# Kernel optimization log

Measured on AMD Instinct MI355X. Metric: run time of the kernel, lower is better.

The kernel has to match this reference:

```python
import jax, jax.numpy as jnp
import numpy as np

NEG = -100000000.0  # NOT_POSSIBLE_TRANSITION
B, T, F, NT = 64, 512, 1024, 50
H = NT + 2  # +2 for start/stop tags
START, STOP = H - 2, H - 1


def setup_inputs() -> dict:
    key = jax.random.key(0)
    k0, k1, k2, k3 = jax.random.split(key, 4)
    features = jax.random.normal(k0, (B, T, F), jnp.float32)
    tags = jax.random.randint(k1, (B, T), 0, NT)
    masks = jnp.ones((B, T), jnp.float32)
    W = jax.random.normal(k2, (H, F), jnp.float32) * 0.02  # nn.Linear weight
    b = jnp.zeros((H,), jnp.float32)                        # nn.Linear bias
    transition = jax.random.normal(k3, (H, H), jnp.float32)
    transition = transition.at[START, :].set(NEG).at[:, STOP].set(NEG)
    return dict(features=features, W=W, b=b, transition=transition,
                masks=masks, tags=tags)


def _forward_algorithm(emit, masks, transition):
    # emit: [B,T,H], masks: [B,T]
    b_, _, h = emit.shape
    init = jnp.full((b_, h), NEG, emit.dtype).at[:, START].set(0.0)

    def step(scores, xs):
        emit_t, mask_t = xs  # [B,H], [B]
        # score_t[b, i] = logsumexp_j(scores[b,j] + transition[i,j] + emit_t[b,i])
        s = scores[:, None, :] + transition[None, :, :] + emit_t[:, :, None]
        s = jax.nn.logsumexp(s, axis=-1)
        m = mask_t[:, None]
        scores = s * m + scores * (1.0 - m)
        return scores, None

    scores, _ = jax.lax.scan(step, init, (emit.transpose(1, 0, 2), masks.T))
    return jax.nn.logsumexp(scores + transition[STOP], axis=-1)  # [B]


def _gold_score(emit, tags, masks, transition):
    b_ = emit.shape[0]
    emit_sc = jnp.take_along_axis(emit, tags[:, :, None], axis=2)[:, :, 0]  # [B,T]
    start = jnp.full((b_, 1), START, tags.dtype)
    tags_ext = jnp.concatenate([start, tags], axis=1)  # [B,T+1]
    trans_sc = transition[tags_ext[:, 1:], tags_ext[:, :-1]]  # [B,T]
    last_pos = masks.sum(axis=1).astype(jnp.int32)  # index into tags_ext
    last_tag = jnp.take_along_axis(tags_ext, last_pos[:, None], axis=1)[:, 0]
    last_score = transition[STOP, last_tag]
    return ((trans_sc + emit_sc) * masks).sum(axis=1) + last_score  # [B]


def reference(features, W, b, transition, masks, tags):
    emit = features @ W.T + b  # [B,T,H]
    fwd = _forward_algorithm(emit, masks, transition)
    gold = _gold_score(emit, tags, masks, transition)
    return (fwd - gold).mean()  # CRF NLL loss (scalar)


if __name__ == "__main__":
    print(reference(**setup_inputs()))
```

## Files before the change

kernel.cpp:

```cpp
#include <hip/hip_runtime.h>
#include <hip/hip_bf16.h>
#include <math.h>


#define NEGV   (-100000000.0f)
#define BB     64
#define TT     512
#define FF     1024
#define HH     52
#define HP     64
#define S_START 50
#define S_STOP  51
#define NCH    32
#define CLEN   (TT / NCH)

typedef __bf16 bf16x8 __attribute__((ext_vector_type(8)));
typedef __bf16 bf16x4 __attribute__((ext_vector_type(4)));
typedef float  f32x4  __attribute__((ext_vector_type(4)));

#define WS_CHUNK  0u
#define WS_WBF    33554432u
#define WS_EXPT   33685504u
#define WS_GOLD   33693696u
#define WS_CEXP   33693952u

__global__ __launch_bounds__(256) void k_prep(const float* __restrict__ W,
                                              const float* __restrict__ trans,
                                              __bf16* __restrict__ wbf,
                                              __bf16* __restrict__ expT,
                                              float* __restrict__ gold) {
  int n = blockIdx.x;
  if (n == 0) {
    if (threadIdx.x < BB) gold[threadIdx.x] = 0.0f;
    for (int idx = threadIdx.x; idx < 4096; idx += 256) {
      int m = idx >> 6, k = idx & 63;
      float tv = (k >= HH) ? NEGV : ((m >= HH) ? 0.0f : trans[m * HH + k]);
      expT[idx] = (__bf16)__expf(tv);
    }
  }
  for (int k = threadIdx.x; k < FF; k += 256) {
    float v = (n < HH) ? W[n * FF + k] : 0.0f;
    wbf[n * FF + k] = (__bf16)v;
  }
}

__global__ __launch_bounds__(256, 2) void k_scan(const float* __restrict__ feat,
                                                 const __bf16* __restrict__ wbf,
                                                 const __bf16* __restrict__ expT,
                                                 const float* __restrict__ bias,
                                                 const float* __restrict__ trans,
                                                 const float* __restrict__ masks,
                                                 const int* __restrict__ tags,
                                                 __bf16* __restrict__ chunks,
                                                 float* __restrict__ cexp,
                                                 float* __restrict__ gold) {
  const int tid = threadIdx.x;
  const int wv = tid >> 6;
  const int l  = tid & 63;
  const int lm = l & 15;
  const int q  = l >> 4;
  const int chunk = blockIdx.x * 4 + wv;
  const int b = chunk >> 5, c = chunk & 31;

  __shared__ __align__(16) __bf16 PTall[4][64 * 72];
  __shared__ __align__(16) __bf16 Eall[4][CLEN * 64];
  __bf16* pt = PTall[wv];
  __bf16* el = Eall[wv];

  const float* fbase = feat + ((size_t)(b * TT + c * CLEN)) * FF;
  const float* arow  = fbase + (size_t)lm * FF + q * 8;

  f32x4 apre[4][2];
#pragma unroll
  for (int s = 0; s < 4; ++s)
#pragma unroll
    for (int h = 0; h < 2; ++h)
      apre[s][h] = *(const f32x4*)(arow + s * 32 + h * 4);

  bf16x8 bcur[4];
#pragma unroll
  for (int nt = 0; nt < 4; ++nt)
    bcur[nt] = *(const bf16x8*)(wbf + (size_t)(nt * 16 + lm) * FF + q * 8);

  f32x4 acc[4] = {};

#pragma unroll
  for (int kt = 0; kt < 32; ++kt) {
    const int st = kt & 3;
    bf16x8 af;
#pragma unroll
    for (int j = 0; j < 4; ++j) {
      af[j]     = (__bf16)apre[st][0][j];
      af[4 + j] = (__bf16)apre[st][1][j];
    }
    if (kt + 4 < 32) {
#pragma unroll
      for (int h = 0; h < 2; ++h)
        apre[st][h] = *(const f32x4*)(arow + (kt + 4) * 32 + h * 4);
    }
    bf16x8 bnx[4];
    if (kt + 1 < 32) {
#pragma unroll
      for (int nt = 0; nt < 4; ++nt)
        bnx[nt] = *(const bf16x8*)(wbf + (size_t)(nt * 16 + lm) * FF + (kt + 1) * 32 + q * 8);
    }
#pragma unroll
    for (int nt = 0; nt < 4; ++nt)
      acc[nt] = __builtin_amdgcn_mfma_f32_16x16x32_bf16(af, bcur[nt], acc[nt], 0, 0, 0);
    if (kt + 1 < 32) {
#pragma unroll
      for (int nt = 0; nt < 4; ++nt) bcur[nt] = bnx[nt];
    }
  }

#pragma unroll
  for (int nt = 0; nt < 4; ++nt) {
    int n = nt * 16 + lm;
    float bn = (n < HH) ? bias[n] : 0.0f;
#pragma unroll
    for (int rr = 0; rr < 4; ++rr)
      el[(q * 4 + rr) * 64 + n] = (__bf16)(acc[nt][rr] + bn);
  }

  float mreg = (l < CLEN) ? masks[b * TT + c * CLEN + l] : 1.0f;
  int cur = (l < CLEN) ? tags[b * TT + c * CLEN + l] : 0;
  int prev = __shfl_up(cur, 1);
  if (l == 0) prev = (c == 0) ? S_START : tags[b * TT + c * CLEN - 1];
  float gp = 0.0f;
  if (l < CLEN) {
    float e  = (float)el[l * 64 + cur];
    float tr = trans[cur * HH + prev];
    gp = (e + tr) * mreg;
  }
#pragma unroll
  for (int d = 1; d < 64; d <<= 1) gp += __shfl_xor(gp, d);
  if (l == 0) atomicAdd(&gold[b], gp);

  bf16x8 afrag[4][2];
#pragma unroll
  for (int mt = 0; mt < 4; ++mt)
#pragma unroll
    for (int kk = 0; kk < 2; ++kk)
      afrag[mt][kk] = *(const bf16x8*)&expT[(mt * 16 + lm) * 64 + kk * 32 + q * 8];

  for (int idx = l; idx < 4096; idx += 64) {
    int n = idx >> 6, mm = idx & 63;
    pt[n * 72 + mm] = (__bf16)((n == mm) ? 1.0f : 0.0f);
  }

  int eacc = 0, rpend = 0;
  const float LOG2E = 1.4426950408889634f;

  for (int t = 0; t < CLEN; ++t) {
    float mcur = __shfl(mreg, t);
    if (mcur != 0.0f) {
      float sh = (float)(7 + rpend);
      eacc += 7 + rpend;
      rpend = 0;
      float s[4][4];
#pragma unroll
      for (int mt = 0; mt < 4; ++mt) {
        bf16x4 em4 = *(const bf16x4*)&el[t * 64 + mt * 16 + q * 4];
#pragma unroll
        for (int rr = 0; rr < 4; ++rr)
          s[mt][rr] = __builtin_amdgcn_exp2f(fmaf((float)em4[rr], LOG2E, -sh));
      }

      bf16x8 bfr[2][4];
#pragma unroll
      for (int kk = 0; kk < 2; ++kk)
#pragma unroll
        for (int nt = 0; nt < 4; ++nt)
          bfr[kk][nt] = *(const bf16x8*)&pt[(nt * 16 + lm) * 72 + kk * 32 + q * 8];

      const bool trk = ((t & 7) == 7) && (t != CLEN - 1);
      float lmax = 0.0f;
      f32x4 zero = {};
#pragma unroll
      for (int mt = 0; mt < 4; ++mt) {
#pragma unroll
        for (int nt = 0; nt < 4; ++nt) {
          f32x4 a = __builtin_amdgcn_mfma_f32_16x16x32_bf16(afrag[mt][0], bfr[0][nt], zero, 0, 0, 0);
          a = __builtin_amdgcn_mfma_f32_16x16x32_bf16(afrag[mt][1], bfr[1][nt], a, 0, 0, 0);
          bf16x4 w4;
#pragma unroll
          for (int rr = 0; rr < 4; ++rr) {
            float v = a[rr] * s[mt][rr];
            if (trk) lmax = fmaxf(lmax, v);
            w4[rr] = (__bf16)v;
          }
          *(bf16x4*)&pt[(nt * 16 + lm) * 72 + mt * 16 + q * 4] = w4;
        }
      }
      if (trk) {
#pragma unroll
        for (int d = 1; d < 64; d <<= 1) lmax = fmaxf(lmax, __shfl_xor(lmax, d));
        rpend = ilogbf(lmax);
      }
    }
  }

  __bf16* cb = chunks + (size_t)chunk * 4096;
#pragma unroll
  for (int it = 0; it < 8; ++it) {
    bf16x8 v;
#pragma unroll
    for (int e = 0; e < 8; ++e) v[e] = pt[(it * 8 + e) * 72 + l];
    *(bf16x8*)&cb[it * 512 + l * 8] = v;
  }
  if (l == 0) cexp[chunk] = (float)eacc;
}

__global__ __launch_bounds__(64) void k_combine(const __bf16* __restrict__ chunks,
                                                const float* __restrict__ cexp,
                                                const float* __restrict__ trans,
                                                const float* __restrict__ masks,
                                                const int* __restrict__ tags,
                                                const float* __restrict__ gold,
                                                float* __restrict__ out) {
  const int b = blockIdx.x;
  const int l = threadIdx.x;
  __shared__ __align__(16) float vsh[64];
  float v = (l == S_START) ? 1.0f : 0.0f;
  float esum = 0.0f;
  const float LN2 = 0.6931471805599453f;

  float msum = 0.0f;
  for (int t = l; t < TT; t += 64) msum += masks[b * TT + t];

  const __bf16* base = chunks + ((size_t)(b * NCH)) * 4096;

  bf16x8 pf[4][8];
#pragma unroll
  for (int p = 0; p < 4; ++p)
#pragma unroll
    for (int it = 0; it < 8; ++it)
      pf[p][it] = *(const bf16x8*)&base[(size_t)p * 4096 + it * 512 + l * 8];

#pragma unroll
  for (int cc = 0; cc < NCH; ++cc) {
    vsh[l] = v;
    __syncthreads();
    float u = 0.0f;
#pragma unroll
    for (int it = 0; it < 8; ++it) {
      bf16x8 m8 = pf[cc & 3][it];
      f32x4 va = *(const f32x4*)&vsh[it * 8];
      f32x4 vb = *(const f32x4*)&vsh[it * 8 + 4];
      u += (float)m8[0] * va[0] + (float)m8[1] * va[1]
         + (float)m8[2] * va[2] + (float)m8[3] * va[3]
         + (float)m8[4] * vb[0] + (float)m8[5] * vb[1]
         + (float)m8[6] * vb[2] + (float)m8[7] * vb[3];
    }
    if (cc + 4 < NCH) {
#pragma unroll
      for (int it = 0; it < 8; ++it)
        pf[cc & 3][it] = *(const bf16x8*)&base[(size_t)(cc + 4) * 4096 + it * 512 + l * 8];
    }
    esum += cexp[b * NCH + cc] * LN2;
    float mxx = u;
#pragma unroll
    for (int d = 1; d < 64; d <<= 1) mxx = fmaxf(mxx, __shfl_xor(mxx, d));
    if (mxx > 0.0f) {
      int ee = ilogbf(mxx);
      u = ldexpf(u, -ee);
      esum += (float)ee * LN2;
    }
    v = u;
    __syncthreads();
  }

  float ts = (l < HH) ? trans[S_STOP * HH + l] : NEGV;
  float contrib = v * __expf(ts);
#pragma unroll
  for (int d = 1; d < 64; d <<= 1) {
    contrib += __shfl_xor(contrib, d);
    msum += __shfl_xor(msum, d);
  }
  if (l == 0) {
    int lp = (int)(msum + 0.5f);
    int lt = (lp == 0) ? S_START : tags[b * TT + lp - 1];
    float goldb = gold[b] + trans[S_STOP * HH + lt];
    float fwd = __logf(contrib) + esum;
    atomicAdd(out, (fwd - goldb) * (1.0f / 64.0f));
  }
}

extern "C" void kernel_launch(void* const* d_in, const int* in_sizes, int n_in,
                              void* d_out, int out_size, void* d_ws, size_t ws_size,
                              hipStream_t stream) {
  (void)in_sizes; (void)n_in; (void)out_size; (void)ws_size;
  const float* feat  = (const float*)d_in[0];
  const float* W     = (const float*)d_in[1];
  const float* bias  = (const float*)d_in[2];
  const float* trans = (const float*)d_in[3];
  const float* masks = (const float*)d_in[4];
  const int*   tags  = (const int*)d_in[5];

  char* ws = (char*)d_ws;
  __bf16* chunks = (__bf16*)(ws + WS_CHUNK);
  __bf16* wbf    = (__bf16*)(ws + WS_WBF);
  __bf16* expT   = (__bf16*)(ws + WS_EXPT);
  float*  gold   = (float*)(ws + WS_GOLD);
  float*  cexp   = (float*)(ws + WS_CEXP);

  hipMemsetAsync(d_out, 0, sizeof(float), stream);
  k_prep<<<HP, 256, 0, stream>>>(W, trans, wbf, expT, gold);
  k_scan<<<(BB * NCH) / 4, 256, 0, stream>>>(feat, wbf, expT, bias, trans, masks,
                                             tags, chunks, cexp, gold);
  k_combine<<<BB, 64, 0, stream>>>(chunks, cexp, trans, masks, tags, gold, (float*)d_out);
}
```

Before: 269.2 us.

## Split each scan chunk across two waves in K and in transfer-matrix columns

Each chunk is now processed by two wavefronts instead of one. They split the feature GEMM along K and reduce the partial sums through shared memory. In the chunk scan each wave owns half of the columns of the transfer-matrix product. Each half keeps its own exponent accumulator, and the combine kernel reconciles the two exponents per chunk by rescaling the vector. This doubles the parallelism and halves the serial per-wave work for the latency-bound scan, at the cost of extra barriers, a renormalisation only at t==7, and possibly more range risk in the bf16 products.

```diff
diff --git a/kernel.cpp b/kernel.cpp
--- a/kernel.cpp
+++ b/kernel.cpp
@@ -19,10 +19,10 @@
 typedef float  f32x4  __attribute__((ext_vector_type(4)));
 
 #define WS_CHUNK  0u
-#define WS_WBF    33554432u
-#define WS_EXPT   33685504u
-#define WS_GOLD   33693696u
-#define WS_CEXP   33693952u
+#define WS_CEXP2  16777216u
+#define WS_WBF    16793600u
+#define WS_EXPT   16924672u
+#define WS_GOLD   16932864u
 
 __global__ __launch_bounds__(256) void k_prep(const float* __restrict__ W,
                                               const float* __restrict__ trans,
@@ -44,7 +44,7 @@
   }
 }
 
-__global__ __launch_bounds__(256, 2) void k_scan(const float* __restrict__ feat,
+__global__ __launch_bounds__(256, 4) void k_scan(const float* __restrict__ feat,
                                                  const __bf16* __restrict__ wbf,
                                                  const __bf16* __restrict__ expT,
                                                  const float* __restrict__ bias,
@@ -52,40 +52,43 @@
                                                  const float* __restrict__ masks,
                                                  const int* __restrict__ tags,
                                                  __bf16* __restrict__ chunks,
-                                                 float* __restrict__ cexp,
+                                                 float* __restrict__ cexp2,
                                                  float* __restrict__ gold) {
   const int tid = threadIdx.x;
   const int wv = tid >> 6;
   const int l  = tid & 63;
   const int lm = l & 15;
   const int q  = l >> 4;
-  const int chunk = blockIdx.x * 4 + wv;
+  const int ck = wv >> 1;
+  const int h  = wv & 1;
+  const int chunk = blockIdx.x * 2 + ck;
   const int b = chunk >> 5, c = chunk & 31;
 
-  __shared__ __align__(16) __bf16 PTall[4][64 * 72];
-  __shared__ __align__(16) __bf16 Eall[4][CLEN * 64];
-  __bf16* pt = PTall[wv];
-  __bf16* el = Eall[wv];
+  __shared__ __align__(16) __bf16 PTall[2][64 * 72];
+  __shared__ __align__(16) __bf16 Eall[2][CLEN * 64];
+  __bf16* pt = PTall[ck];
+  __bf16* el = Eall[ck];
+  float*  pstage = (float*)pt;
 
   const float* fbase = feat + ((size_t)(b * TT + c * CLEN)) * FF;
-  const float* arow  = fbase + (size_t)lm * FF + q * 8;
+  const float* arow  = fbase + (size_t)lm * FF + h * 512 + q * 8;
 
   f32x4 apre[4][2];
 #pragma unroll
   for (int s = 0; s < 4; ++s)
 #pragma unroll
-    for (int h = 0; h < 2; ++h)
-      apre[s][h] = *(const f32x4*)(arow + s * 32 + h * 4);
+    for (int hh = 0; hh < 2; ++hh)
+      apre[s][hh] = *(const f32x4*)(arow + s * 32 + hh * 4);
 
   bf16x8 bcur[4];
 #pragma unroll
   for (int nt = 0; nt < 4; ++nt)
-    bcur[nt] = *(const bf16x8*)(wbf + (size_t)(nt * 16 + lm) * FF + q * 8);
+    bcur[nt] = *(const bf16x8*)(wbf + (size_t)(nt * 16 + lm) * FF + h * 512 + q * 8);
 
   f32x4 acc[4] = {};
 
 #pragma unroll
-  for (int kt = 0; kt < 32; ++kt) {
+  for (int kt = 0; kt < 16; ++kt) {
     const int st = kt & 3;
     bf16x8 af;
 #pragma unroll
@@ -93,48 +96,58 @@
       af[j]     = (__bf16)apre[st][0][j];
       af[4 + j] = (__bf16)apre[st][1][j];
     }
-    if (kt + 4 < 32) {
-#pragma unroll
-      for (int h = 0; h < 2; ++h)
-        apre[st][h] = *(const f32x4*)(arow + (kt + 4) * 32 + h * 4);
+    if (kt + 4 < 16) {
+#pragma unroll
+      for (int hh = 0; hh < 2; ++hh)
+        apre[st][hh] = *(const f32x4*)(arow + (kt + 4) * 32 + hh * 4);
     }
     bf16x8 bnx[4];
-    if (kt + 1 < 32) {
+    if (kt + 1 < 16) {
 #pragma unroll
       for (int nt = 0; nt < 4; ++nt)
-        bnx[nt] = *(const bf16x8*)(wbf + (size_t)(nt * 16 + lm) * FF + (kt + 1) * 32 + q * 8);
+        bnx[nt] = *(const bf16x8*)(wbf + (size_t)(nt * 16 + lm) * FF + h * 512 + (kt + 1) * 32 + q * 8);
     }
 #pragma unroll
     for (int nt = 0; nt < 4; ++nt)
       acc[nt] = __builtin_amdgcn_mfma_f32_16x16x32_bf16(af, bcur[nt], acc[nt], 0, 0, 0);
-    if (kt + 1 < 32) {
+    if (kt + 1 < 16) {
 #pragma unroll
       for (int nt = 0; nt < 4; ++nt) bcur[nt] = bnx[nt];
     }
   }
 
 #pragma unroll
-  for (int nt = 0; nt < 4; ++nt) {
-    int n = nt * 16 + lm;
-    float bn = (n < HH) ? bias[n] : 0.0f;
+  for (int nt = 0; nt < 4; ++nt)
 #pragma unroll
     for (int rr = 0; rr < 4; ++rr)
-      el[(q * 4 + rr) * 64 + n] = (__bf16)(acc[nt][rr] + bn);
-  }
+      pstage[h * 1024 + (q * 4 + rr) * 64 + nt * 16 + lm] = acc[nt][rr];
+  __syncthreads();
+
+  {
+    float bl = (l < HH) ? bias[l] : 0.0f;
+#pragma unroll
+    for (int i2 = 0; i2 < 8; ++i2) {
+      int t = i2 * 2 + h;
+      el[t * 64 + l] = (__bf16)(pstage[t * 64 + l] + pstage[1024 + t * 64 + l] + bl);
+    }
+  }
+  __syncthreads();
 
   float mreg = (l < CLEN) ? masks[b * TT + c * CLEN + l] : 1.0f;
-  int cur = (l < CLEN) ? tags[b * TT + c * CLEN + l] : 0;
-  int prev = __shfl_up(cur, 1);
-  if (l == 0) prev = (c == 0) ? S_START : tags[b * TT + c * CLEN - 1];
-  float gp = 0.0f;
-  if (l < CLEN) {
-    float e  = (float)el[l * 64 + cur];
-    float tr = trans[cur * HH + prev];
-    gp = (e + tr) * mreg;
-  }
-#pragma unroll
-  for (int d = 1; d < 64; d <<= 1) gp += __shfl_xor(gp, d);
-  if (l == 0) atomicAdd(&gold[b], gp);
+  if (h == 0) {
+    int cur = (l < CLEN) ? tags[b * TT + c * CLEN + l] : 0;
+    int prev = __shfl_up(cur, 1);
+    if (l == 0) prev = (c == 0) ? S_START : tags[b * TT + c * CLEN - 1];
+    float gp = 0.0f;
+    if (l < CLEN) {
+      float e  = (float)el[l * 64 + cur];
+      float tr = trans[cur * HH + prev];
+      gp = (e + tr) * mreg;
+    }
+#pragma unroll
+    for (int d = 1; d < 64; d <<= 1) gp += __shfl_xor(gp, d);
+    if (l == 0) atomicAdd(&gold[b], gp);
+  }
 
   bf16x8 afrag[4][2];
 #pragma unroll
@@ -143,9 +156,10 @@
     for (int kk = 0; kk < 2; ++kk)
       afrag[mt][kk] = *(const bf16x8*)&expT[(mt * 16 + lm) * 64 + kk * 32 + q * 8];
 
-  for (int idx = l; idx < 4096; idx += 64) {
-    int n = idx >> 6, mm = idx & 63;
-    pt[n * 72 + mm] = (__bf16)((n == mm) ? 1.0f : 0.0f);
+#pragma unroll
+  for (int r = 0; r < 32; ++r) {
+    int j = h * 32 + r;
+    pt[j * 72 + l] = (__bf16)((j == l) ? 1.0f : 0.0f);
   }
 
   int eacc = 0, rpend = 0;
@@ -166,20 +180,20 @@
           s[mt][rr] = __builtin_amdgcn_exp2f(fmaf((float)em4[rr], LOG2E, -sh));
       }
 
-      bf16x8 bfr[2][4];
+      bf16x8 bfr[2][2];
 #pragma unroll
       for (int kk = 0; kk < 2; ++kk)
 #pragma unroll
-        for (int nt = 0; nt < 4; ++nt)
-          bfr[kk][nt] = *(const bf16x8*)&pt[(nt * 16 + lm) * 72 + kk * 32 + q * 8];
-
-      const bool trk = ((t & 7) == 7) && (t != CLEN - 1);
+        for (int nt = 0; nt < 2; ++nt)
+          bfr[kk][nt] = *(const bf16x8*)&pt[((h * 2 + nt) * 16 + lm) * 72 + kk * 32 + q * 8];
+
+      const bool trk = (t == 7);
       float lmax = 0.0f;
       f32x4 zero = {};
 #pragma unroll
       for (int mt = 0; mt < 4; ++mt) {
 #pragma unroll
-        for (int nt = 0; nt < 4; ++nt) {
+        for (int nt = 0; nt < 2; ++nt) {
           f32x4 a = __builtin_amdgcn_mfma_f32_16x16x32_bf16(afrag[mt][0], bfr[0][nt], zero, 0, 0, 0);
           a = __builtin_amdgcn_mfma_f32_16x16x32_bf16(afrag[mt][1], bfr[1][nt], a, 0, 0, 0);
           bf16x4 w4;
@@ -189,30 +203,31 @@
             if (trk) lmax = fmaxf(lmax, v);
             w4[rr] = (__bf16)v;
           }
-          *(bf16x4*)&pt[(nt * 16 + lm) * 72 + mt * 16 + q * 4] = w4;
+          *(bf16x4*)&pt[((h * 2 + nt) * 16 + lm) * 72 + mt * 16 + q * 4] = w4;
         }
       }
       if (trk) {
 #pragma unroll
         for (int d = 1; d < 64; d <<= 1) lmax = fmaxf(lmax, __shfl_xor(lmax, d));
-        rpend = ilogbf(lmax);
+        if (lmax > 0.0f) rpend = ilogbf(lmax);
       }
     }
   }
 
   __bf16* cb = chunks + (size_t)chunk * 4096;
 #pragma unroll
-  for (int it = 0; it < 8; ++it) {
+  for (int i4 = 0; i4 < 4; ++i4) {
+    int it = h * 4 + i4;
     bf16x8 v;
 #pragma unroll
     for (int e = 0; e < 8; ++e) v[e] = pt[(it * 8 + e) * 72 + l];
     *(bf16x8*)&cb[it * 512 + l * 8] = v;
   }
-  if (l == 0) cexp[chunk] = (float)eacc;
+  if (l == 0) cexp2[chunk * 2 + h] = (float)eacc;
 }
 
 __global__ __launch_bounds__(64) void k_combine(const __bf16* __restrict__ chunks,
-                                                const float* __restrict__ cexp,
+                                                const float* __restrict__ cexp2,
                                                 const float* __restrict__ trans,
                                                 const float* __restrict__ masks,
                                                 const int* __restrict__ tags,
@@ -239,7 +254,11 @@
 
 #pragma unroll
   for (int cc = 0; cc < NCH; ++cc) {
-    vsh[l] = v;
+    float E0 = cexp2[(b * NCH + cc) * 2];
+    float E1 = cexp2[(b * NCH + cc) * 2 + 1];
+    float Em = fmaxf(E0, E1);
+    int   dl = (int)(((l < 32) ? E0 : E1) - Em);
+    vsh[l] = ldexpf(v, dl);
     __syncthreads();
     float u = 0.0f;
 #pragma unroll
@@ -257,7 +276,7 @@
       for (int it = 0; it < 8; ++it)
         pf[cc & 3][it] = *(const bf16x8*)&base[(size_t)(cc + 4) * 4096 + it * 512 + l * 8];
     }
-    esum += cexp[b * NCH + cc] * LN2;
+    esum += Em * LN2;
     float mxx = u;
 #pragma unroll
     for (int d = 1; d < 64; d <<= 1) mxx = fmaxf(mxx, __shfl_xor(mxx, d));
@@ -299,14 +318,14 @@
 
   char* ws = (char*)d_ws;
   __bf16* chunks = (__bf16*)(ws + WS_CHUNK);
+  float*  cexp2  = (float*)(ws + WS_CEXP2);
   __bf16* wbf    = (__bf16*)(ws + WS_WBF);
   __bf16* expT   = (__bf16*)(ws + WS_EXPT);
   float*  gold   = (float*)(ws + WS_GOLD);
-  float*  cexp   = (float*)(ws + WS_CEXP);
 
   hipMemsetAsync(d_out, 0, sizeof(float), stream);
   k_prep<<<HP, 256, 0, stream>>>(W, trans, wbf, expT, gold);
-  k_scan<<<(BB * NCH) / 4, 256, 0, stream>>>(feat, wbf, expT, bias, trans, masks,
-                                             tags, chunks, cexp, gold);
-  k_combine<<<BB, 64, 0, stream>>>(chunks, cexp, trans, masks, tags, gold, (float*)d_out);
+  k_scan<<<(BB * NCH) / 2, 256, 0, stream>>>(feat, wbf, expT, bias, trans, masks,
+                                             tags, chunks, cexp2, gold);
+  k_combine<<<BB, 64, 0, stream>>>(chunks, cexp2, trans, masks, tags, gold, (float*)d_out);
 }
```

After: 268.6 us. Within noise of the previous version (-0.2%).

## Stage feature tiles through double-buffered LDS with coalesced block-wide loads

Applied to the files above, without the earlier changes.

The emission GEMM now has all 256 threads load each 64-row by 128-column feature tile with coalesced float4 reads. The tile is converted to bf16 into a double-buffered LDS area that is later reused as the per-wave scan matrix. This replaces the per-lane strided fp32 register prefetch and lets the occupancy hint rise from 2 to 3 blocks per CU. The cost is a block-wide barrier per stage. Workspace offsets are compacted, and ilogbf is guarded against a non-positive max.

```diff
diff --git a/kernel.cpp b/kernel.cpp
--- a/kernel.cpp
+++ b/kernel.cpp
@@ -19,10 +19,12 @@
 typedef float  f32x4  __attribute__((ext_vector_type(4)));
 
 #define WS_CHUNK  0u
-#define WS_WBF    33554432u
-#define WS_EXPT   33685504u
-#define WS_GOLD   33693696u
-#define WS_CEXP   33693952u
+#define WS_CEXP   16777216u
+#define WS_WBF    16793600u
+#define WS_EXPT   16924672u
+#define WS_GOLD   16932864u
+
+#define ASTRIDE 132
 
 __global__ __launch_bounds__(256) void k_prep(const float* __restrict__ W,
                                               const float* __restrict__ trans,
@@ -44,7 +46,7 @@
   }
 }
 
-__global__ __launch_bounds__(256, 2) void k_scan(const float* __restrict__ feat,
+__global__ __launch_bounds__(256, 3) void k_scan(const float* __restrict__ feat,
                                                  const __bf16* __restrict__ wbf,
                                                  const __bf16* __restrict__ expT,
                                                  const float* __restrict__ bias,
@@ -62,20 +64,28 @@
   const int chunk = blockIdx.x * 4 + wv;
   const int b = chunk >> 5, c = chunk & 31;
 
-  __shared__ __align__(16) __bf16 PTall[4][64 * 72];
+  __shared__ __align__(16) __bf16 POOL[4 * 64 * 72];
   __shared__ __align__(16) __bf16 Eall[4][CLEN * 64];
-  __bf16* pt = PTall[wv];
   __bf16* el = Eall[wv];
 
-  const float* fbase = feat + ((size_t)(b * TT + c * CLEN)) * FF;
-  const float* arow  = fbase + (size_t)lm * FF + q * 8;
-
-  f32x4 apre[4][2];
-#pragma unroll
-  for (int s = 0; s < 4; ++s)
-#pragma unroll
-    for (int h = 0; h < 2; ++h)
-      apre[s][h] = *(const f32x4*)(arow + s * 32 + h * 4);
+  const float* fblock = feat + (size_t)(blockIdx.x * 64) * FF;
+  const int srow = tid >> 5;
+  const int scol = (tid & 31) * 4;
+  __bf16* AS0 = POOL;
+  __bf16* AS1 = POOL + 64 * ASTRIDE;
+
+  f32x4 sreg[8];
+#pragma unroll
+  for (int j = 0; j < 8; ++j)
+    sreg[j] = *(const f32x4*)(fblock + (size_t)(j * 8 + srow) * FF + scol);
+#pragma unroll
+  for (int j = 0; j < 8; ++j) {
+    bf16x4 w;
+#pragma unroll
+    for (int i = 0; i < 4; ++i) w[i] = (__bf16)sreg[j][i];
+    *(bf16x4*)&AS0[(j * 8 + srow) * ASTRIDE + scol] = w;
+  }
+  __syncthreads();
 
   bf16x8 bcur[4];
 #pragma unroll
@@ -85,32 +95,47 @@
   f32x4 acc[4] = {};
 
 #pragma unroll
-  for (int kt = 0; kt < 32; ++kt) {
-    const int st = kt & 3;
-    bf16x8 af;
-#pragma unroll
-    for (int j = 0; j < 4; ++j) {
-      af[j]     = (__bf16)apre[st][0][j];
-      af[4 + j] = (__bf16)apre[st][1][j];
-    }
-    if (kt + 4 < 32) {
-#pragma unroll
-      for (int h = 0; h < 2; ++h)
-        apre[st][h] = *(const f32x4*)(arow + (kt + 4) * 32 + h * 4);
-    }
-    bf16x8 bnx[4];
-    if (kt + 1 < 32) {
+  for (int s = 0; s < 8; ++s) {
+    __bf16* cur = (s & 1) ? AS1 : AS0;
+    __bf16* nxt = (s & 1) ? AS0 : AS1;
+    if (s < 7) {
+#pragma unroll
+      for (int j = 0; j < 8; ++j)
+        sreg[j] = *(const f32x4*)(fblock + (size_t)(j * 8 + srow) * FF + (s + 1) * 128 + scol);
+    }
+#pragma unroll
+    for (int k2 = 0; k2 < 4; ++k2) {
+      const int fk = s * 4 + k2;
+      const __bf16* ap = &cur[(wv * 16 + lm) * ASTRIDE + k2 * 32 + q * 8];
+      bf16x4 a0 = *(const bf16x4*)ap;
+      bf16x4 a1 = *(const bf16x4*)(ap + 4);
+      bf16x8 af;
+      af[0] = a0[0]; af[1] = a0[1]; af[2] = a0[2]; af[3] = a0[3];
+      af[4] = a1[0]; af[5] = a1[1]; af[6] = a1[2]; af[7] = a1[3];
+      bf16x8 bnx[4];
+      if (fk + 1 < 32) {
+#pragma unroll
+        for (int nt = 0; nt < 4; ++nt)
+          bnx[nt] = *(const bf16x8*)(wbf + (size_t)(nt * 16 + lm) * FF + (fk + 1) * 32 + q * 8);
+      }
 #pragma unroll
       for (int nt = 0; nt < 4; ++nt)
-        bnx[nt] = *(const bf16x8*)(wbf + (size_t)(nt * 16 + lm) * FF + (kt + 1) * 32 + q * 8);
-    }
-#pragma unroll
-    for (int nt = 0; nt < 4; ++nt)
-      acc[nt] = __builtin_amdgcn_mfma_f32_16x16x32_bf16(af, bcur[nt], acc[nt], 0, 0, 0);
-    if (kt + 1 < 32) {
-#pragma unroll
-      for (int nt = 0; nt < 4; ++nt) bcur[nt] = bnx[nt];
-    }
+        acc[nt] = __builtin_amdgcn_mfma_f32_16x16x32_bf16(af, bcur[nt], acc[nt], 0, 0, 0);
+      if (fk + 1 < 32) {
+#pragma unroll
+        for (int nt = 0; nt < 4; ++nt) bcur[nt] = bnx[nt];
+      }
+    }
+    if (s < 7) {
+#pragma unroll
+      for (int j = 0; j < 8; ++j) {
+        bf16x4 w;
+#pragma unroll
+        for (int i = 0; i < 4; ++i) w[i] = (__bf16)sreg[j][i];
+        *(bf16x4*)&nxt[(j * 8 + srow) * ASTRIDE + scol] = w;
+      }
+    }
+    __syncthreads();
   }
 
 #pragma unroll
@@ -123,18 +148,20 @@
   }
 
   float mreg = (l < CLEN) ? masks[b * TT + c * CLEN + l] : 1.0f;
-  int cur = (l < CLEN) ? tags[b * TT + c * CLEN + l] : 0;
-  int prev = __shfl_up(cur, 1);
+  int cur_t = (l < CLEN) ? tags[b * TT + c * CLEN + l] : 0;
+  int prev = __shfl_up(cur_t, 1);
   if (l == 0) prev = (c == 0) ? S_START : tags[b * TT + c * CLEN - 1];
   float gp = 0.0f;
   if (l < CLEN) {
-    float e  = (float)el[l * 64 + cur];
-    float tr = trans[cur * HH + prev];
+    float e  = (float)el[l * 64 + cur_t];
+    float tr = trans[cur_t * HH + prev];
     gp = (e + tr) * mreg;
   }
 #pragma unroll
   for (int d = 1; d < 64; d <<= 1) gp += __shfl_xor(gp, d);
   if (l == 0) atomicAdd(&gold[b], gp);
+
+  __bf16* pt = POOL + wv * (64 * 72);
 
   bf16x8 afrag[4][2];
 #pragma unroll
@@ -195,7 +222,7 @@
       if (trk) {
 #pragma unroll
         for (int d = 1; d < 64; d <<= 1) lmax = fmaxf(lmax, __shfl_xor(lmax, d));
-        rpend = ilogbf(lmax);
+        if (lmax > 0.0f) rpend = ilogbf(lmax);
       }
     }
   }
@@ -299,10 +326,10 @@
 
   char* ws = (char*)d_ws;
   __bf16* chunks = (__bf16*)(ws + WS_CHUNK);
+  float*  cexp   = (float*)(ws + WS_CEXP);
   __bf16* wbf    = (__bf16*)(ws + WS_WBF);
   __bf16* expT   = (__bf16*)(ws + WS_EXPT);
   float*  gold   = (float*)(ws + WS_GOLD);
-  float*  cexp   = (float*)(ws + WS_CEXP);
 
   hipMemsetAsync(d_out, 0, sizeof(float), stream);
   k_prep<<<HP, 256, 0, stream>>>(W, trans, wbf, expT, gold);
```

Measured after the change: 274.6 us. 2.0% more time.

## Split chunk combine into parallel group matrix products then short serial pass

Applied to the files above, without the earlier changes.

The sequential combine over 32 chunk transfer matrices per batch becomes two stages. First, 256 blocks each multiply 8 consecutive chunk matrices together with MFMA and renormalise by a power of two. Then a short serial pass walks only 4 group matrices per batch. This shortens the serial dependency chain in the combine, which ran with only 64 single-wave blocks, at the cost of an extra launch and more matrix-matrix work in bf16. The second-stage loop also drops its __syncthreads calls, which is safe with one wave per block, and a zero-max guard is added before ilogbf in the scan.

```diff
diff --git a/kernel.cpp b/kernel.cpp
--- a/kernel.cpp
+++ b/kernel.cpp
@@ -13,16 +13,20 @@
 #define S_STOP  51
 #define NCH    32
 #define CLEN   (TT / NCH)
+#define GRP    8
+#define NGRP   (NCH / GRP)
 
 typedef __bf16 bf16x8 __attribute__((ext_vector_type(8)));
 typedef __bf16 bf16x4 __attribute__((ext_vector_type(4)));
 typedef float  f32x4  __attribute__((ext_vector_type(4)));
 
 #define WS_CHUNK  0u
-#define WS_WBF    33554432u
-#define WS_EXPT   33685504u
-#define WS_GOLD   33693696u
-#define WS_CEXP   33693952u
+#define WS_CEXP   16777216u
+#define WS_GBUF   16785408u
+#define WS_GCEXP  18882560u
+#define WS_WBF    18883584u
+#define WS_EXPT   19014656u
+#define WS_GOLD   19022848u
 
 __global__ __launch_bounds__(256) void k_prep(const float* __restrict__ W,
                                               const float* __restrict__ trans,
@@ -195,7 +199,7 @@
       if (trk) {
 #pragma unroll
         for (int d = 1; d < 64; d <<= 1) lmax = fmaxf(lmax, __shfl_xor(lmax, d));
-        rpend = ilogbf(lmax);
+        if (lmax > 0.0f) rpend = ilogbf(lmax);
       }
     }
   }
@@ -211,13 +215,93 @@
   if (l == 0) cexp[chunk] = (float)eacc;
 }
 
-__global__ __launch_bounds__(64) void k_combine(const __bf16* __restrict__ chunks,
-                                                const float* __restrict__ cexp,
-                                                const float* __restrict__ trans,
-                                                const float* __restrict__ masks,
-                                                const int* __restrict__ tags,
-                                                const float* __restrict__ gold,
-                                                float* __restrict__ out) {
+__global__ __launch_bounds__(64) void k_ga(const __bf16* __restrict__ chunks,
+                                           const float* __restrict__ cexp,
+                                           __bf16* __restrict__ gbuf,
+                                           float* __restrict__ gcexp) {
+  const int g  = blockIdx.x;
+  const int b  = g >> 2, qq = g & 3;
+  const int l  = threadIdx.x;
+  const int lm = l & 15;
+  const int q  = l >> 4;
+
+  __shared__ __align__(16) __bf16 ptq[64 * 72];
+  const __bf16* mbase = chunks + ((size_t)(b * NCH + qq * GRP)) * 4096;
+
+#pragma unroll
+  for (int it = 0; it < 8; ++it) {
+    bf16x8 mv = *(const bf16x8*)&mbase[it * 512 + l * 8];
+#pragma unroll
+    for (int e = 0; e < 8; ++e) ptq[(it * 8 + e) * 72 + l] = mv[e];
+  }
+
+#pragma unroll
+  for (int j = 1; j < GRP; ++j) {
+    const __bf16* mj = mbase + (size_t)j * 4096;
+    bf16x8 af[4][2];
+#pragma unroll
+    for (int mt = 0; mt < 4; ++mt)
+#pragma unroll
+      for (int kk = 0; kk < 2; ++kk)
+        af[mt][kk] = *(const bf16x8*)&mj[(kk * 4 + q) * 512 + (mt * 16 + lm) * 8];
+    bf16x8 bfr[2][4];
+#pragma unroll
+    for (int kk = 0; kk < 2; ++kk)
+#pragma unroll
+      for (int nt = 0; nt < 4; ++nt)
+        bfr[kk][nt] = *(const bf16x8*)&ptq[(nt * 16 + lm) * 72 + kk * 32 + q * 8];
+    f32x4 zero = {};
+#pragma unroll
+    for (int mt = 0; mt < 4; ++mt) {
+#pragma unroll
+      for (int nt = 0; nt < 4; ++nt) {
+        f32x4 a = __builtin_amdgcn_mfma_f32_16x16x32_bf16(af[mt][0], bfr[0][nt], zero, 0, 0, 0);
+        a = __builtin_amdgcn_mfma_f32_16x16x32_bf16(af[mt][1], bfr[1][nt], a, 0, 0, 0);
+        bf16x4 w4;
+#pragma unroll
+        for (int rr = 0; rr < 4; ++rr) w4[rr] = (__bf16)a[rr];
+        *(bf16x4*)&ptq[(nt * 16 + lm) * 72 + mt * 16 + q * 4] = w4;
+      }
+    }
+  }
+
+  float vals[8][8];
+  float lmax = 0.0f;
+#pragma unroll
+  for (int it = 0; it < 8; ++it)
+#pragma unroll
+    for (int e = 0; e < 8; ++e) {
+      float x = (float)ptq[(it * 8 + e) * 72 + l];
+      vals[it][e] = x;
+      lmax = fmaxf(lmax, x);
+    }
+#pragma unroll
+  for (int d = 1; d < 64; d <<= 1) lmax = fmaxf(lmax, __shfl_xor(lmax, d));
+  int ee = (lmax > 0.0f) ? ilogbf(lmax) : 0;
+  float sc = ldexpf(1.0f, -ee);
+  __bf16* gb = gbuf + (size_t)g * 4096;
+#pragma unroll
+  for (int it = 0; it < 8; ++it) {
+    bf16x8 w;
+#pragma unroll
+    for (int e = 0; e < 8; ++e) w[e] = (__bf16)(vals[it][e] * sc);
+    *(bf16x8*)&gb[it * 512 + l * 8] = w;
+  }
+  if (l == 0) {
+    float s = (float)ee;
+#pragma unroll
+    for (int c = 0; c < GRP; ++c) s += cexp[b * NCH + qq * GRP + c];
+    gcexp[g] = s;
+  }
+}
+
+__global__ __launch_bounds__(64) void k_gb(const __bf16* __restrict__ gbuf,
+                                           const float* __restrict__ gcexp,
+                                           const float* __restrict__ trans,
+                                           const float* __restrict__ masks,
+                                           const int* __restrict__ tags,
+                                           const float* __restrict__ gold,
+                                           float* __restrict__ out) {
   const int b = blockIdx.x;
   const int l = threadIdx.x;
   __shared__ __align__(16) float vsh[64];
@@ -228,23 +312,20 @@
   float msum = 0.0f;
   for (int t = l; t < TT; t += 64) msum += masks[b * TT + t];
 
-  const __bf16* base = chunks + ((size_t)(b * NCH)) * 4096;
-
-  bf16x8 pf[4][8];
-#pragma unroll
-  for (int p = 0; p < 4; ++p)
+  bf16x8 pf[NGRP][8];
+#pragma unroll
+  for (int p = 0; p < NGRP; ++p)
 #pragma unroll
     for (int it = 0; it < 8; ++it)
-      pf[p][it] = *(const bf16x8*)&base[(size_t)p * 4096 + it * 512 + l * 8];
-
-#pragma unroll
-  for (int cc = 0; cc < NCH; ++cc) {
+      pf[p][it] = *(const bf16x8*)&gbuf[((size_t)(b * NGRP + p)) * 4096 + it * 512 + l * 8];
+
+#pragma unroll
+  for (int g = 0; g < NGRP; ++g) {
     vsh[l] = v;
-    __syncthreads();
     float u = 0.0f;
 #pragma unroll
     for (int it = 0; it < 8; ++it) {
-      bf16x8 m8 = pf[cc & 3][it];
+      bf16x8 m8 = pf[g][it];
       f32x4 va = *(const f32x4*)&vsh[it * 8];
       f32x4 vb = *(const f32x4*)&vsh[it * 8 + 4];
       u += (float)m8[0] * va[0] + (float)m8[1] * va[1]
@@ -252,12 +333,7 @@
          + (float)m8[4] * vb[0] + (float)m8[5] * vb[1]
          + (float)m8[6] * vb[2] + (float)m8[7] * vb[3];
     }
-    if (cc + 4 < NCH) {
-#pragma unroll
-      for (int it = 0; it < 8; ++it)
-        pf[cc & 3][it] = *(const bf16x8*)&base[(size_t)(cc + 4) * 4096 + it * 512 + l * 8];
-    }
-    esum += cexp[b * NCH + cc] * LN2;
+    esum += gcexp[b * NGRP + g] * LN2;
     float mxx = u;
 #pragma unroll
     for (int d = 1; d < 64; d <<= 1) mxx = fmaxf(mxx, __shfl_xor(mxx, d));
@@ -267,7 +343,6 @@
       esum += (float)ee * LN2;
     }
     v = u;
-    __syncthreads();
   }
 
   float ts = (l < HH) ? trans[S_STOP * HH + l] : NEGV;
@@ -299,14 +374,17 @@
 
   char* ws = (char*)d_ws;
   __bf16* chunks = (__bf16*)(ws + WS_CHUNK);
+  float*  cexp   = (float*)(ws + WS_CEXP);
+  __bf16* gbuf   = (__bf16*)(ws + WS_GBUF);
+  float*  gcexp  = (float*)(ws + WS_GCEXP);
   __bf16* wbf    = (__bf16*)(ws + WS_WBF);
   __bf16* expT   = (__bf16*)(ws + WS_EXPT);
   float*  gold   = (float*)(ws + WS_GOLD);
-  float*  cexp   = (float*)(ws + WS_CEXP);
 
   hipMemsetAsync(d_out, 0, sizeof(float), stream);
   k_prep<<<HP, 256, 0, stream>>>(W, trans, wbf, expT, gold);
   k_scan<<<(BB * NCH) / 4, 256, 0, stream>>>(feat, wbf, expT, bias, trans, masks,
                                              tags, chunks, cexp, gold);
-  k_combine<<<BB, 64, 0, stream>>>(chunks, cexp, trans, masks, tags, gold, (float*)d_out);
-}
+  k_ga<<<BB * NGRP, 64, 0, stream>>>(chunks, cexp, gbuf, gcexp);
+  k_gb<<<BB, 64, 0, stream>>>(gbuf, gcexp, trans, masks, tags, gold, (float*)d_out);
+}
```

New measurement: 257.7 us. -4.3%, faster.
